# Optimization experiments

Measured on AMD Instinct MI355X. Metric: run time of the kernel, lower is better.

Reference implementation:

```python
import jax, jax.numpy as jnp
import numpy as np

NUM_POINTS = 200000
IN_FEATURES = 128
OUT_FEATURES = 128
NUM_RELATIONS = 128
NUM_BLOCKS = 16
IN_BLOCK = IN_FEATURES // NUM_BLOCKS   # 8
OUT_BLOCK = OUT_FEATURES // NUM_BLOCKS  # 8


def setup_inputs() -> dict:
    key = jax.random.key(0)
    k1, k2, k3 = jax.random.split(key, 3)
    x = jax.random.normal(k1, (NUM_POINTS, IN_FEATURES), dtype=jnp.float32)
    # glorot-uniform init of the per-relation block-diagonal weights
    blocks = jax.nn.initializers.glorot_uniform()(
        k2, (NUM_RELATIONS, NUM_BLOCKS, IN_BLOCK, OUT_BLOCK), jnp.float32)
    rel = jax.random.randint(k3, (NUM_POINTS,), 0, NUM_RELATIONS)
    return {"x": x, "blocks": blocks, "rel": rel}


def reference(x, blocks, rel):
    # x: [p, num_blocks*in_block]; blocks: [R, nb, ib, ob]; rel: [p] int
    p = x.shape[0]
    R, nb, ib, ob = blocks.shape
    x_by_block = x.reshape(p, nb, ib)                 # [p, nb, ib]
    relation_blocks = blocks[rel]                     # gather: [p, nb, ib, ob]
    transformed = jnp.einsum('pnio,pni->pno', relation_blocks, x_by_block)
    return transformed.reshape(p, nb * ob)            # [p, out_features]
```

## Files before the change

### kernel.cpp

```cpp
#include <hip/hip_runtime.h>


#define SEGS 16
#define NR 128

__global__ __launch_bounds__(256) void k_hist(const int* __restrict__ rel,
                                              int* __restrict__ counts, int npoints)
{
    __shared__ int h[NR];
    for (int i = threadIdx.x; i < NR; i += 256) h[i] = 0;
    __syncthreads();
    for (int p = blockIdx.x * 256 + threadIdx.x; p < npoints; p += gridDim.x * 256)
        atomicAdd(&h[rel[p]], 1);
    __syncthreads();
    for (int i = threadIdx.x; i < NR; i += 256)
        if (h[i]) atomicAdd(&counts[i], h[i]);
}

__global__ __launch_bounds__(NR) void k_scan(const int* __restrict__ counts,
                                             int* __restrict__ starts,
                                             int* __restrict__ cursor)
{
    __shared__ int buf[NR];
    int t = threadIdx.x;
    int v = counts[t];
    buf[t] = v;
    __syncthreads();
    #pragma unroll
    for (int off = 1; off < NR; off <<= 1) {
        int y = (t >= off) ? buf[t - off] : 0;
        __syncthreads();
        buf[t] += y;
        __syncthreads();
    }
    int excl = buf[t] - v;
    starts[t] = excl;
    cursor[t] = excl;
}

__global__ __launch_bounds__(256) void k_scatter(const int* __restrict__ rel,
                                                 int* __restrict__ cursor,
                                                 int* __restrict__ perm, int npoints)
{
    __shared__ int cnt[NR], base[NR], rk[NR];
    int chunk = (npoints + gridDim.x - 1) / gridDim.x;
    int lo = blockIdx.x * chunk;
    int hi = min(lo + chunk, npoints);
    for (int i = threadIdx.x; i < NR; i += 256) { cnt[i] = 0; rk[i] = 0; }
    __syncthreads();
    for (int p = lo + threadIdx.x; p < hi; p += 256) atomicAdd(&cnt[rel[p]], 1);
    __syncthreads();
    for (int i = threadIdx.x; i < NR; i += 256)
        base[i] = cnt[i] ? atomicAdd(&cursor[i], cnt[i]) : 0;
    __syncthreads();
    for (int p = lo + threadIdx.x; p < hi; p += 256) {
        int r = rel[p];
        int k = atomicAdd(&rk[r], 1);
        perm[base[r] + k] = p;
    }
}

__global__ __launch_bounds__(256) void k_main(
    const float* __restrict__ x, const float* __restrict__ w,
    const int* __restrict__ starts, const int* __restrict__ counts,
    const int* __restrict__ perm, float* __restrict__ out)
{
    int r   = blockIdx.x >> 4;
    int seg = blockIdx.x & (SEGS - 1);
    int start = starts[r], cnt = counts[r];
    int lo = start + (cnt * seg) / SEGS;
    int hi = start + (cnt * (seg + 1)) / SEGS;
    int scnt = hi - lo;

    int lane = threadIdx.x & 63;
    int wv   = threadIdx.x >> 6;
    int n = lane >> 2, c = lane & 3;

    const float* wb = w + ((size_t)r * 16 + n) * 64 + 2 * c;
    float w0[8], w1[8];
    #pragma unroll
    for (int i = 0; i < 8; ++i) {
        float2 t = *reinterpret_cast<const float2*>(wb + i * 8);
        w0[i] = t.x; w1[i] = t.y;
    }

    int wlo = lo + (scnt * wv) / 4;
    int whi = lo + (scnt * (wv + 1)) / 4;
    int nk  = whi - wlo;

    const int xoff = n * 8;
    const int ooff = n * 8 + 2 * c;

    for (int k0 = 0; k0 < nk; k0 += 64) {
        int nbatch = min(64, nk - k0);
        int pidx = (lane < nbatch) ? perm[wlo + k0 + lane] : 0;

        int    P0[4], P1[4];
        float4 X0[4][2], X1[4][2];

        auto loadg = [&](int j0, int P[4], float4 X[4][2]) {
            #pragma unroll
            for (int u = 0; u < 4; ++u) {
                int j = j0 + u;
                if (j < nbatch) {
                    int p = __builtin_amdgcn_readlane(pidx, j);
                    P[u] = p;
                    const float4* xv = reinterpret_cast<const float4*>(
                        x + (size_t)p * 128 + xoff);
                    X[u][0] = xv[0];
                    X[u][1] = xv[1];
                } else {
                    P[u] = -1;
                }
            }
        };
        auto computeg = [&](const int P[4], const float4 X[4][2]) {
            #pragma unroll
            for (int u = 0; u < 4; ++u) {
                if (P[u] < 0) continue;
                float4 xa = X[u][0], xb = X[u][1];
                float a0 = 0.f, a1 = 0.f;
                a0 = fmaf(xa.x, w0[0], a0); a1 = fmaf(xa.x, w1[0], a1);
                a0 = fmaf(xa.y, w0[1], a0); a1 = fmaf(xa.y, w1[1], a1);
                a0 = fmaf(xa.z, w0[2], a0); a1 = fmaf(xa.z, w1[2], a1);
                a0 = fmaf(xa.w, w0[3], a0); a1 = fmaf(xa.w, w1[3], a1);
                a0 = fmaf(xb.x, w0[4], a0); a1 = fmaf(xb.x, w1[4], a1);
                a0 = fmaf(xb.y, w0[5], a0); a1 = fmaf(xb.y, w1[5], a1);
                a0 = fmaf(xb.z, w0[6], a0); a1 = fmaf(xb.z, w1[6], a1);
                a0 = fmaf(xb.w, w0[7], a0); a1 = fmaf(xb.w, w1[7], a1);
                *reinterpret_cast<float2*>(out + (size_t)P[u] * 128 + ooff) =
                    make_float2(a0, a1);
            }
        };

        loadg(0, P0, X0);
        int j0 = 0;
        while (j0 < nbatch) {
            loadg(j0 + 4, P1, X1);
            computeg(P0, X0);
            j0 += 4;
            if (j0 >= nbatch) break;
            loadg(j0 + 4, P0, X0);
            computeg(P1, X1);
            j0 += 4;
        }
    }
}

__global__ __launch_bounds__(256) void brl_kernel(
    const float* __restrict__ x, const float* __restrict__ w,
    const int* __restrict__ rel, float* __restrict__ out, int npoints)
{
    int tid = blockIdx.x * 256 + threadIdx.x;
    int p = tid >> 4;
    if (p >= npoints) return;
    int n = tid & 15;
    int r = rel[p];
    const float4* xv = reinterpret_cast<const float4*>(x + (size_t)p * 128 + n * 8);
    float4 x0 = xv[0], x1 = xv[1];
    float xf[8] = {x0.x, x0.y, x0.z, x0.w, x1.x, x1.y, x1.z, x1.w};
    const float4* wv = reinterpret_cast<const float4*>(w + ((size_t)r * 16 + n) * 64);
    float acc[8] = {0.f,0.f,0.f,0.f,0.f,0.f,0.f,0.f};
    #pragma unroll
    for (int i = 0; i < 8; ++i) {
        float4 w0 = wv[2*i], w1 = wv[2*i+1];
        float wf[8] = {w0.x,w0.y,w0.z,w0.w,w1.x,w1.y,w1.z,w1.w};
        #pragma unroll
        for (int o = 0; o < 8; ++o) acc[o] = fmaf(xf[i], wf[o], acc[o]);
    }
    float4* ov = reinterpret_cast<float4*>(out + (size_t)p * 128 + n * 8);
    ov[0] = make_float4(acc[0], acc[1], acc[2], acc[3]);
    ov[1] = make_float4(acc[4], acc[5], acc[6], acc[7]);
}

extern "C" void kernel_launch(void* const* d_in, const int* in_sizes, int n_in,
                              void* d_out, int out_size, void* d_ws, size_t ws_size,
                              hipStream_t stream) {
    const float* x   = (const float*)d_in[0];
    const float* w   = (const float*)d_in[1];
    const int*   rel = (const int*)d_in[2];
    float*       out = (float*)d_out;

    int npoints = in_sizes[2];
    int R = in_sizes[1] / 1024;

    size_t need = (size_t)(3 * NR + npoints) * sizeof(int);
    if (R != NR || ws_size < need) {
        int total = npoints * 16;
        brl_kernel<<<(total + 255) / 256, 256, 0, stream>>>(x, w, rel, out, npoints);
        return;
    }

    int* counts = (int*)d_ws;
    int* starts = counts + NR;
    int* cursor = starts + NR;
    int* perm   = cursor + NR;

    hipMemsetAsync(counts, 0, NR * sizeof(int), stream);
    k_hist   <<<128, 256, 0, stream>>>(rel, counts, npoints);
    k_scan   <<<1, NR, 0, stream>>>(counts, starts, cursor);
    k_scatter<<<128, 256, 0, stream>>>(rel, cursor, perm, npoints);
    k_main   <<<NR * SEGS, 256, 0, stream>>>(x, w, starts, counts, perm, out);
}
```

Measured before the change: 213.4 us.

## Replace sort-by-relation pipeline with single fused kernel using LDS-resident weights

Drops the histogram/scan/scatter permutation pipeline and the gather-based main kernel. In their place is one kernel that stages a quarter of all relation weights (4 of 16 blocks, all 128 relations, 128KB) in LDS with an XOR swizzle. Each thread then streams points in their natural order, looking up weights by relation from LDS and prefetching the next point's x. This removes four launches, the perm indirection and the non-coalesced gather traffic. In exchange it needs 128KB of LDS per block (one block per CU) and a full weight reload in every block, and LDS reads are divergent because neighbouring points have random relations.

```diff
diff --git a/kernel.cpp b/kernel.cpp
--- a/kernel.cpp
+++ b/kernel.cpp
@@ -1,149 +1,76 @@
 #include <hip/hip_runtime.h>
 
 
-#define SEGS 16
-#define NR 128
+__global__ __launch_bounds__(1024) void k_fused(
+    const float* __restrict__ x, const float* __restrict__ w,
+    const int* __restrict__ rel, float* __restrict__ out, int npoints)
+{
+    __shared__ float4 wlds[4][128][16];
 
-__global__ __launch_bounds__(256) void k_hist(const int* __restrict__ rel,
-                                              int* __restrict__ counts, int npoints)
-{
-    __shared__ int h[NR];
-    for (int i = threadIdx.x; i < NR; i += 256) h[i] = 0;
+    const int q = blockIdx.x >> 6;
+    const int b = blockIdx.x & 63;
+
+    const float4* wsrc = reinterpret_cast<const float4*>(w);
+    #pragma unroll
+    for (int j = 0; j < 8; ++j) {
+        int f  = threadIdx.x + j * 1024;
+        int r  = f >> 6;
+        int lo = f & 63;
+        int nl = lo >> 4;
+        int k  = f & 15;
+        wlds[nl][r][k ^ (r & 15)] = wsrc[r * 256 + q * 64 + lo];
+    }
     __syncthreads();
-    for (int p = blockIdx.x * 256 + threadIdx.x; p < npoints; p += gridDim.x * 256)
-        atomicAdd(&h[rel[p]], 1);
-    __syncthreads();
-    for (int i = threadIdx.x; i < NR; i += 256)
-        if (h[i]) atomicAdd(&counts[i], h[i]);
-}
 
-__global__ __launch_bounds__(NR) void k_scan(const int* __restrict__ counts,
-                                             int* __restrict__ starts,
-                                             int* __restrict__ cursor)
-{
-    __shared__ int buf[NR];
-    int t = threadIdx.x;
-    int v = counts[t];
-    buf[t] = v;
-    __syncthreads();
-    #pragma unroll
-    for (int off = 1; off < NR; off <<= 1) {
-        int y = (t >= off) ? buf[t - off] : 0;
-        __syncthreads();
-        buf[t] += y;
-        __syncthreads();
-    }
-    int excl = buf[t] - v;
-    starts[t] = excl;
-    cursor[t] = excl;
-}
+    const int nl = threadIdx.x & 3;
+    const int pt = threadIdx.x >> 2;
+    const int chunk = (npoints + 63) >> 6;
+    const int plo = b * chunk;
+    const int phi = min(plo + chunk, npoints);
+    const int n  = q * 4 + nl;
 
-__global__ __launch_bounds__(256) void k_scatter(const int* __restrict__ rel,
-                                                 int* __restrict__ cursor,
-                                                 int* __restrict__ perm, int npoints)
-{
-    __shared__ int cnt[NR], base[NR], rk[NR];
-    int chunk = (npoints + gridDim.x - 1) / gridDim.x;
-    int lo = blockIdx.x * chunk;
-    int hi = min(lo + chunk, npoints);
-    for (int i = threadIdx.x; i < NR; i += 256) { cnt[i] = 0; rk[i] = 0; }
-    __syncthreads();
-    for (int p = lo + threadIdx.x; p < hi; p += 256) atomicAdd(&cnt[rel[p]], 1);
-    __syncthreads();
-    for (int i = threadIdx.x; i < NR; i += 256)
-        base[i] = cnt[i] ? atomicAdd(&cursor[i], cnt[i]) : 0;
-    __syncthreads();
-    for (int p = lo + threadIdx.x; p < hi; p += 256) {
-        int r = rel[p];
-        int k = atomicAdd(&rk[r], 1);
-        perm[base[r] + k] = p;
-    }
-}
+    int p = plo + pt;
+    if (p >= phi) return;
 
-__global__ __launch_bounds__(256) void k_main(
-    const float* __restrict__ x, const float* __restrict__ w,
-    const int* __restrict__ starts, const int* __restrict__ counts,
-    const int* __restrict__ perm, float* __restrict__ out)
-{
-    int r   = blockIdx.x >> 4;
-    int seg = blockIdx.x & (SEGS - 1);
-    int start = starts[r], cnt = counts[r];
-    int lo = start + (cnt * seg) / SEGS;
-    int hi = start + (cnt * (seg + 1)) / SEGS;
-    int scnt = hi - lo;
+    const float* xb = x + n * 8;
+    float*       ob = out + n * 8;
 
-    int lane = threadIdx.x & 63;
-    int wv   = threadIdx.x >> 6;
-    int n = lane >> 2, c = lane & 3;
+    int r = rel[p];
+    const float4* xv = reinterpret_cast<const float4*>(xb + (size_t)p * 128);
+    float4 x0 = xv[0], x1 = xv[1];
 
-    const float* wb = w + ((size_t)r * 16 + n) * 64 + 2 * c;
-    float w0[8], w1[8];
-    #pragma unroll
-    for (int i = 0; i < 8; ++i) {
-        float2 t = *reinterpret_cast<const float2*>(wb + i * 8);
-        w0[i] = t.x; w1[i] = t.y;
-    }
+    while (true) {
+        int pn = p + 256;
+        int pc = pn < phi ? pn : (phi - 1);
+        int rn = rel[pc];
+        const float4* xnv = reinterpret_cast<const float4*>(xb + (size_t)pc * 128);
+        float4 xn0 = xnv[0], xn1 = xnv[1];
 
-    int wlo = lo + (scnt * wv) / 4;
-    int whi = lo + (scnt * (wv + 1)) / 4;
-    int nk  = whi - wlo;
+        const int s = r & 15;
+        const float4* wr = wlds[nl][r];
+        float xf[8] = {x0.x, x0.y, x0.z, x0.w, x1.x, x1.y, x1.z, x1.w};
+        float a0 = 0.f, a1 = 0.f, a2 = 0.f, a3 = 0.f;
+        float a4 = 0.f, a5 = 0.f, a6 = 0.f, a7 = 0.f;
+        #pragma unroll
+        for (int i = 0; i < 8; ++i) {
+            float4 wA = wr[(2 * i)     ^ s];
+            float4 wB = wr[(2 * i + 1) ^ s];
+            float xi = xf[i];
+            a0 = fmaf(xi, wA.x, a0);
+            a1 = fmaf(xi, wA.y, a1);
+            a2 = fmaf(xi, wA.z, a2);
+            a3 = fmaf(xi, wA.w, a3);
+            a4 = fmaf(xi, wB.x, a4);
+            a5 = fmaf(xi, wB.y, a5);
+            a6 = fmaf(xi, wB.z, a6);
+            a7 = fmaf(xi, wB.w, a7);
+        }
+        float4* ov = reinterpret_cast<float4*>(ob + (size_t)p * 128);
+        ov[0] = make_float4(a0, a1, a2, a3);
+        ov[1] = make_float4(a4, a5, a6, a7);
 
-    const int xoff = n * 8;
-    const int ooff = n * 8 + 2 * c;
-
-    for (int k0 = 0; k0 < nk; k0 += 64) {
-        int nbatch = min(64, nk - k0);
-        int pidx = (lane < nbatch) ? perm[wlo + k0 + lane] : 0;
-
-        int    P0[4], P1[4];
-        float4 X0[4][2], X1[4][2];
-
-        auto loadg = [&](int j0, int P[4], float4 X[4][2]) {
-            #pragma unroll
-            for (int u = 0; u < 4; ++u) {
-                int j = j0 + u;
-                if (j < nbatch) {
-                    int p = __builtin_amdgcn_readlane(pidx, j);
-                    P[u] = p;
-                    const float4* xv = reinterpret_cast<const float4*>(
-                        x + (size_t)p * 128 + xoff);
-                    X[u][0] = xv[0];
-                    X[u][1] = xv[1];
-                } else {
-                    P[u] = -1;
-                }
-            }
-        };
-        auto computeg = [&](const int P[4], const float4 X[4][2]) {
-            #pragma unroll
-            for (int u = 0; u < 4; ++u) {
-                if (P[u] < 0) continue;
-                float4 xa = X[u][0], xb = X[u][1];
-                float a0 = 0.f, a1 = 0.f;
-                a0 = fmaf(xa.x, w0[0], a0); a1 = fmaf(xa.x, w1[0], a1);
-                a0 = fmaf(xa.y, w0[1], a0); a1 = fmaf(xa.y, w1[1], a1);
-                a0 = fmaf(xa.z, w0[2], a0); a1 = fmaf(xa.z, w1[2], a1);
-                a0 = fmaf(xa.w, w0[3], a0); a1 = fmaf(xa.w, w1[3], a1);
-                a0 = fmaf(xb.x, w0[4], a0); a1 = fmaf(xb.x, w1[4], a1);
-                a0 = fmaf(xb.y, w0[5], a0); a1 = fmaf(xb.y, w1[5], a1);
-                a0 = fmaf(xb.z, w0[6], a0); a1 = fmaf(xb.z, w1[6], a1);
-                a0 = fmaf(xb.w, w0[7], a0); a1 = fmaf(xb.w, w1[7], a1);
-                *reinterpret_cast<float2*>(out + (size_t)P[u] * 128 + ooff) =
-                    make_float2(a0, a1);
-            }
-        };
-
-        loadg(0, P0, X0);
-        int j0 = 0;
-        while (j0 < nbatch) {
-            loadg(j0 + 4, P1, X1);
-            computeg(P0, X0);
-            j0 += 4;
-            if (j0 >= nbatch) break;
-            loadg(j0 + 4, P0, X0);
-            computeg(P1, X1);
-            j0 += 4;
-        }
+        if (pn >= phi) break;
+        p = pn; r = rn; x0 = xn0; x1 = xn1;
     }
 }
 
@@ -160,11 +87,11 @@
     float4 x0 = xv[0], x1 = xv[1];
     float xf[8] = {x0.x, x0.y, x0.z, x0.w, x1.x, x1.y, x1.z, x1.w};
     const float4* wv = reinterpret_cast<const float4*>(w + ((size_t)r * 16 + n) * 64);
-    float acc[8] = {0.f,0.f,0.f,0.f,0.f,0.f,0.f,0.f};
+    float acc[8] = {0.f, 0.f, 0.f, 0.f, 0.f, 0.f, 0.f, 0.f};
     #pragma unroll
     for (int i = 0; i < 8; ++i) {
-        float4 w0 = wv[2*i], w1 = wv[2*i+1];
-        float wf[8] = {w0.x,w0.y,w0.z,w0.w,w1.x,w1.y,w1.z,w1.w};
+        float4 w0 = wv[2 * i], w1 = wv[2 * i + 1];
+        float wf[8] = {w0.x, w0.y, w0.z, w0.w, w1.x, w1.y, w1.z, w1.w};
         #pragma unroll
         for (int o = 0; o < 8; ++o) acc[o] = fmaf(xf[i], wf[o], acc[o]);
     }
@@ -184,21 +111,10 @@
     int npoints = in_sizes[2];
     int R = in_sizes[1] / 1024;
 
-    size_t need = (size_t)(3 * NR + npoints) * sizeof(int);
-    if (R != NR || ws_size < need) {
+    if (R == 128 && in_sizes[0] == npoints * 128) {
+        k_fused<<<256, 1024, 0, stream>>>(x, w, rel, out, npoints);
+    } else {
         int total = npoints * 16;
         brl_kernel<<<(total + 255) / 256, 256, 0, stream>>>(x, w, rel, out, npoints);
-        return;
     }
-
-    int* counts = (int*)d_ws;
-    int* starts = counts + NR;
-    int* cursor = starts + NR;
-    int* perm   = cursor + NR;
-
-    hipMemsetAsync(counts, 0, NR * sizeof(int), stream);
-    k_hist   <<<128, 256, 0, stream>>>(rel, counts, npoints);
-    k_scan   <<<1, NR, 0, stream>>>(counts, starts, cursor);
-    k_scatter<<<128, 256, 0, stream>>>(rel, cursor, perm, npoints);
-    k_main   <<<NR * SEGS, 256, 0, stream>>>(x, w, starts, counts, perm, out);
 }
```

Measured after the change: 198.2 us. 1.08x faster.
